# Optimization experiments

Measured on AMD Instinct MI355X. Metric: run time of the kernel, lower is better.

Reference implementation:

```python
import jax, jax.numpy as jnp
import numpy as np

D_MODEL = 1024
D_K = 64
D_V = 64
N_HEADS = 16
LN_EPS = 1e-5


def setup_inputs() -> dict:
    key = jax.random.key(0)
    ks = jax.random.split(key, 9)
    B, S = 2, 2048
    scale = 0.02
    return {
        "input_Q": jax.random.normal(ks[0], (B, S, D_MODEL), dtype=jnp.float32),
        "input_K": jax.random.normal(ks[1], (B, S, D_MODEL), dtype=jnp.float32),
        "input_V": jax.random.normal(ks[2], (B, S, D_MODEL), dtype=jnp.float32),
        "W_Q": jax.random.normal(ks[3], (D_MODEL, N_HEADS * D_K), dtype=jnp.float32) * scale,
        "W_K": jax.random.normal(ks[4], (D_MODEL, N_HEADS * D_K), dtype=jnp.float32) * scale,
        "W_V": jax.random.normal(ks[5], (D_MODEL, N_HEADS * D_V), dtype=jnp.float32) * scale,
        "W_O": jax.random.normal(ks[6], (N_HEADS * D_V, D_MODEL), dtype=jnp.float32) * scale,
        "ln_gamma": jnp.ones((D_MODEL,), dtype=jnp.float32),
        "ln_beta": jnp.zeros((D_MODEL,), dtype=jnp.float32),
    }


def reference(input_Q, input_K, input_V, W_Q, W_K, W_V, W_O, ln_gamma, ln_beta):
    B, Lq, _ = input_Q.shape
    Lk = input_K.shape[1]
    # projections -> [B, H, L, d]
    Q = (input_Q @ W_Q).reshape(B, Lq, N_HEADS, D_K).transpose(0, 2, 1, 3)
    K = (input_K @ W_K).reshape(B, Lk, N_HEADS, D_K).transpose(0, 2, 1, 3)
    V = (input_V @ W_V).reshape(B, Lk, N_HEADS, D_V).transpose(0, 2, 1, 3)
    # scores: [B, H, Lq, Lk]
    scores = jnp.einsum("bhqd,bhkd->bhqk", Q, K) / jnp.sqrt(jnp.float32(D_K))
    # NOTE: source uses nn.Softmax(dim=1) -> softmax over the HEADS axis (faithful quirk)
    attn = jax.nn.softmax(scores, axis=1)
    context = jnp.einsum("bhqk,bhkv->bhqv", attn, V)
    context = context.transpose(0, 2, 1, 3).reshape(B, Lq, N_HEADS * D_V)
    output = context @ W_O
    # residual + LayerNorm over last dim
    x = output + input_Q
    mu = jnp.mean(x, axis=-1, keepdims=True)
    var = jnp.mean(jnp.square(x - mu), axis=-1, keepdims=True)
    return (x - mu) / jnp.sqrt(var + LN_EPS) * ln_gamma + ln_beta
```

## Files before the change

### kernel.cpp

```cpp
#include <hip/hip_runtime.h>
#include <cstdint>
#include <cstddef>

#define DM 1024
#define HEADS 16
#define DHEAD 64
#define SEQ 2048
#define BATCH 2

typedef __bf16 bf16x8 __attribute__((ext_vector_type(8)));
typedef float  f32x4  __attribute__((ext_vector_type(4)));
typedef unsigned short u16;
typedef unsigned int u32;
typedef u16 u16x8 __attribute__((ext_vector_type(8)));
typedef u16 u16x4 __attribute__((ext_vector_type(4)));

__device__ __forceinline__ float bf2f(u16 u){
    union { u32 i; float f; } v; v.i = ((u32)u) << 16; return v.f;
}
__device__ __forceinline__ u16 f2bf(float f){
    union { float f; u32 i; } v; v.f = f;
    u32 r = v.i + 0x7FFF + ((v.i >> 16) & 1);
    return (u16)(r >> 16);
}
__device__ __forceinline__ u16 f2bf_rhu(float f){
    union { float f; u32 i; } v; v.f = f;
    return (u16)((v.i + 0x8000u) >> 16);
}
__device__ __forceinline__ void gload16(const u16* g, u16* l){
    __builtin_amdgcn_global_load_lds(
        (const __attribute__((address_space(1))) u32*)g,
        (__attribute__((address_space(3))) u32*)l, 16, 0, 0);
}

__global__ void k_probe(const u16* __restrict__ q, int* __restrict__ hdr){
    if (threadIdx.x == 0 && blockIdx.x == 0){
        int cnt = 0;
        for (int i = 0; i < 256; i += 2){
            int e = (q[i] >> 7) & 0xFF;
            if (e >= 90 && e <= 141) cnt++;
        }
        hdr[0] = (cnt >= 64) ? 1 : 0;
        #pragma unroll
        for (int c = 1; c <= 8; c++) hdr[c] = 0;
    }
}

__global__ __launch_bounds__(256) void k_cvt3(const void* __restrict__ s0,
                                              const void* __restrict__ s1,
                                              const void* __restrict__ s2,
                                              u16* __restrict__ dstbase,
                                              const int* __restrict__ flag, int n){
    int z = blockIdx.y;
    const void* src = (z == 0) ? s0 : ((z == 1) ? s1 : s2);
    u16* dst = dstbase + (size_t)z * n;
    int i = (blockIdx.x * 256 + threadIdx.x) * 8;
    if (i >= n) return;
    if (*flag){
        *(u16x8*)&dst[i] = *(const u16x8*)((const u16*)src + i);
    } else {
        const float* s = (const float*)src + i;
        u16x8 o;
        #pragma unroll
        for (int j = 0; j < 8; j++) o[j] = f2bf(s[j]);
        *(u16x8*)&dst[i] = o;
    }
}

__global__ void k_tcvt4(const void* __restrict__ w0, const void* __restrict__ w1,
                        const void* __restrict__ w2, const void* __restrict__ w3,
                        u16* __restrict__ dstbase,
                        const int* __restrict__ flag, int R, int C){
    __shared__ u16 tile[32][33];
    int z = blockIdx.z;
    const void* src = (z == 0) ? w0 : ((z == 1) ? w1 : ((z == 2) ? w2 : w3));
    u16* dst = dstbase + (size_t)z * R * C;
    bool isbf = (*flag != 0);
    int c0 = blockIdx.x * 32, r0 = blockIdx.y * 32;
    int tx = threadIdx.x, ty = threadIdx.y;
    #pragma unroll
    for (int i = 0; i < 32; i += 8){
        size_t idx = (size_t)(r0 + ty + i) * C + c0 + tx;
        tile[ty + i][tx] = isbf ? ((const u16*)src)[idx] : f2bf(((const float*)src)[idx]);
    }
    __syncthreads();
    #pragma unroll
    for (int i = 0; i < 32; i += 8)
        dst[(size_t)(c0 + ty + i) * R + r0 + tx] = tile[tx][ty + i];
}

__global__ void k_transpose(const u16* __restrict__ src, u16* __restrict__ dst,
                            int R, int C){
    __shared__ u16 tile[32][33];
    size_t boff = (size_t)blockIdx.z * R * C;
    src += boff; dst += boff;
    int c0 = blockIdx.x * 32, r0 = blockIdx.y * 32;
    int tx = threadIdx.x, ty = threadIdx.y;
    #pragma unroll
    for (int i = 0; i < 32; i += 8)
        tile[ty + i][tx] = src[(size_t)(r0 + ty + i) * C + c0 + tx];
    __syncthreads();
    #pragma unroll
    for (int i = 0; i < 32; i += 8)
        dst[(size_t)(c0 + ty + i) * R + r0 + tx] = tile[tx][ty + i];
}

__global__ __launch_bounds__(256, 2) void k_gemm3z(const u16* __restrict__ A0,
                                                   const u16* __restrict__ Bt0,
                                                   u16* __restrict__ C0,
                                                   size_t strA, size_t strB, size_t strC,
                                                   int M, int N, int K){
    __shared__ u16 lsA[128 * 32];
    __shared__ u16 lsB[128 * 32];
    int z = blockIdx.z;
    const u16* A  = A0  + strA * z;
    const u16* Bt = Bt0 + strB * z;
    u16* C = C0 + strC * z;
    int m0 = blockIdx.y * 128, n0 = blockIdx.x * 128;
    int t = threadIdx.x, lane = t & 63, w = t >> 6;
    int l15 = lane & 15, quad = lane >> 4;
    int wm = (w & 1) * 64, wn = (w >> 1) * 64;
    int r0 = 32 * w + (lane >> 2);
    int r1 = r0 + 16;
    int c0s = (lane & 3) ^ (r0 & 3);
    int c1s = (lane & 3) ^ (r1 & 3);
    u16* dA0 = &lsA[(32 * w) * 32];
    u16* dA1 = &lsA[(32 * w + 16) * 32];
    u16* dB0 = &lsB[(32 * w) * 32];
    u16* dB1 = &lsB[(32 * w + 16) * 32];
    f32x4 acc[4][4] = {};
    for (int k0 = 0; k0 < K; k0 += 32){
        __syncthreads();
        gload16(&A [(size_t)(m0 + r0) * K + k0 + c0s * 8], dA0);
        gload16(&A [(size_t)(m0 + r1) * K + k0 + c1s * 8], dA1);
        gload16(&Bt[(size_t)(n0 + r0) * K + k0 + c0s * 8], dB0);
        gload16(&Bt[(size_t)(n0 + r1) * K + k0 + c1s * 8], dB1);
        __syncthreads();
        bf16x8 af[4], bfr[4];
        #pragma unroll
        for (int i = 0; i < 4; i++){
            int row = wm + i * 16 + l15;
            af[i] = *(const bf16x8*)&lsA[row * 32 + ((quad ^ (row & 3)) * 8)];
        }
        #pragma unroll
        for (int j = 0; j < 4; j++){
            int row = wn + j * 16 + l15;
            bfr[j] = *(const bf16x8*)&lsB[row * 32 + ((quad ^ (row & 3)) * 8)];
        }
        #pragma unroll
        for (int i = 0; i < 4; i++)
            #pragma unroll
            for (int j = 0; j < 4; j++)
                acc[i][j] = __builtin_amdgcn_mfma_f32_16x16x32_bf16(af[i], bfr[j], acc[i][j], 0, 0, 0);
    }
    #pragma unroll
    for (int i = 0; i < 4; i++)
        #pragma unroll
        for (int j = 0; j < 4; j++)
            #pragma unroll
            for (int r = 0; r < 4; r++){
                int m = m0 + wm + i * 16 + quad * 4 + r;
                int n = n0 + wn + j * 16 + l15;
                C[(size_t)m * N + n] = f2bf(acc[i][j][r]);
            }
}

__global__ __launch_bounds__(1024, 4) void k_attn5(const u16* __restrict__ Qp,
                                                   const u16* __restrict__ Kp,
                                                   const u16* __restrict__ Vt,
                                                   u16* __restrict__ c0,
                                                   u16* __restrict__ c1,
                                                   u16* __restrict__ c2,
                                                   u16* __restrict__ c3,
                                                   int* __restrict__ cnt,
                                                   int ncomboM1, int iters){
    __shared__ u16 ebuf[2][16][64][36];
    __shared__ int s_combo, s_slot;
    int t = threadIdx.x;
    if (t == 0){
        int xcc;
        asm volatile("s_getreg_b32 %0, hwreg(HW_REG_XCC_ID)" : "=s"(xcc));
        int start = xcc & ncomboM1;
        int combo = -1, slot = -1;
        for (int a = 0; a <= ncomboM1 && combo < 0; a++){
            int c = (start + a) & ncomboM1;
            int s = atomicAdd(&cnt[c], 1);
            if (s < 32){ combo = c; slot = s; }
        }
        s_combo = combo; s_slot = slot;
    }
    __syncthreads();
    int combo = s_combo;
    if (combo < 0) return;
    int b = combo & 1, chunk = combo >> 1;
    int q0 = s_slot * 64;
    int h = t >> 6, lane = t & 63, l15 = lane & 15, quad = lane >> 4;
    u16* outp = (chunk == 0) ? c0 : ((chunk == 1) ? c1 : ((chunk == 2) ? c2 : c3));
    const float cexp = 0.125f * 1.44269504f;
    int kbeg = chunk * (iters << 5);

    bf16x8 qf[4][2];
    #pragma unroll
    for (int sub = 0; sub < 4; sub++)
        #pragma unroll
        for (int ch = 0; ch < 2; ch++)
            qf[sub][ch] = *(const bf16x8*)&Qp[((size_t)(b * SEQ + q0 + sub * 16 + l15)) * DM
                                             + h * DHEAD + ch * 32 + quad * 8];

    f32x4 oacc[4][4] = {};
    int sq = t >> 4, sku = (t & 15) * 2;

    auto score_phase = [&](int it){
        int k0 = kbeg + (it << 5), bf = it & 1;
        #pragma unroll
        for (int kt = 0; kt < 2; kt++){
            const u16* kb = Kp + ((size_t)(b * SEQ + k0 + kt * 16 + l15)) * DM + h * DHEAD + quad * 8;
            bf16x8 kf0 = *(const bf16x8*)(kb);
            bf16x8 kf1 = *(const bf16x8*)(kb + 32);
            #pragma unroll
            for (int sub = 0; sub < 4; sub++){
                f32x4 sc = {};
                sc = __builtin_amdgcn_mfma_f32_16x16x32_bf16(qf[sub][0], kf0, sc, 0, 0, 0);
                sc = __builtin_amdgcn_mfma_f32_16x16x32_bf16(qf[sub][1], kf1, sc, 0, 0, 0);
                #pragma unroll
                for (int r = 0; r < 4; r++)
                    ebuf[bf][h][sub * 16 + quad * 4 + r][kt * 16 + l15] =
                        f2bf_rhu(exp2f(sc[r] * cexp));
            }
        }
    };

    score_phase(0);
    for (int it = 0; it < iters; it++){
        int bf = it & 1;
        __syncthreads();
        if (it + 1 < iters) score_phase(it + 1);
        {
            u32 ev[16];
            float s0 = 0.f, s1 = 0.f;
            #pragma unroll
            for (int hh = 0; hh < 16; hh++){
                u32 u = *(const u32*)&ebuf[bf][hh][sq][sku];
                ev[hh] = u;
                union { u32 i; float f; } lo, hi;
                lo.i = u << 16; hi.i = u & 0xFFFF0000u;
                s0 += lo.f; s1 += hi.f;
            }
            float r0 = __builtin_amdgcn_rcpf(s0);
            float r1 = __builtin_amdgcn_rcpf(s1);
            #pragma unroll
            for (int hh = 0; hh < 16; hh++){
                union { u32 i; float f; } lo, hi, p0, p1;
                lo.i = ev[hh] << 16; hi.i = ev[hh] & 0xFFFF0000u;
                p0.f = lo.f * r0; p1.f = hi.f * r1;
                *(u32*)&ebuf[bf][hh][sq][sku] =
                    ((p0.i + 0x8000u) >> 16) | ((p1.i + 0x8000u) & 0xFFFF0000u);
            }
        }
        __syncthreads();
        int k0 = kbeg + (it << 5);
        bf16x8 pa[4];
        #pragma unroll
        for (int sub = 0; sub < 4; sub++){
            const u16* pp = &ebuf[bf][h][sub * 16 + l15][quad * 8];
            union { bf16x8 v; u16x4 q[2]; } pu;
            pu.q[0] = *(const u16x4*)pp;
            pu.q[1] = *(const u16x4*)(pp + 4);
            pa[sub] = pu.v;
        }
        #pragma unroll
        for (int vt = 0; vt < 4; vt++){
            bf16x8 vf = *(const bf16x8*)&Vt[((size_t)b * DM + h * DHEAD + vt * 16 + l15) * SEQ
                                            + k0 + quad * 8];
            #pragma unroll
            for (int sub = 0; sub < 4; sub++)
                oacc[sub][vt] = __builtin_amdgcn_mfma_f32_16x16x32_bf16(pa[sub], vf, oacc[sub][vt], 0, 0, 0);
        }
    }
    #pragma unroll
    for (int sub = 0; sub < 4; sub++)
        #pragma unroll
        for (int vt = 0; vt < 4; vt++)
            #pragma unroll
            for (int r = 0; r < 4; r++){
                int q = q0 + sub * 16 + quad * 4 + r;
                int n = h * DHEAD + vt * 16 + l15;
                outp[((size_t)b * SEQ + q) * DM + n] = f2bf(oacc[sub][vt][r]);
            }
}

__global__ __launch_bounds__(256) void k_reduce(const u16* __restrict__ a,
                                                const u16* __restrict__ b,
                                                const u16* __restrict__ c,
                                                const u16* __restrict__ d,
                                                u16* __restrict__ dst, int n, int nch){
    int i = (blockIdx.x * 256 + threadIdx.x) * 8;
    if (i >= n) return;
    u16x8 x = *(const u16x8*)&a[i];
    u16x8 y = *(const u16x8*)&b[i];
    u16x8 o;
    if (nch == 4){
        u16x8 zc = *(const u16x8*)&c[i];
        u16x8 zd = *(const u16x8*)&d[i];
        #pragma unroll
        for (int j = 0; j < 8; j++)
            o[j] = f2bf((bf2f(x[j]) + bf2f(y[j])) + (bf2f(zc[j]) + bf2f(zd[j])));
    } else {
        #pragma unroll
        for (int j = 0; j < 8; j++) o[j] = f2bf(bf2f(x[j]) + bf2f(y[j]));
    }
    *(u16x8*)&dst[i] = o;
}

__global__ __launch_bounds__(256) void k_ln(const u16* __restrict__ O,
                                            const void* __restrict__ Qin,
                                            const void* __restrict__ gamma,
                                            const void* __restrict__ beta,
                                            void* __restrict__ out,
                                            const int* __restrict__ flag){
    __shared__ float red[4][2];
    bool isbf = (*flag != 0);
    int row = blockIdx.x;
    int t = threadIdx.x;
    const u16* op = O + (size_t)row * DM;
    float xv[4];
    float s1 = 0.f, s2 = 0.f;
    #pragma unroll
    for (int i = 0; i < 4; i++){
        int idx = i * 256 + t;
        float q = isbf ? bf2f(((const u16*)Qin)[(size_t)row * DM + idx])
                       : ((const float*)Qin)[(size_t)row * DM + idx];
        float x = bf2f(op[idx]) + q;
        xv[i] = x; s1 += x; s2 += x * x;
    }
    #pragma unroll
    for (int off = 32; off; off >>= 1){
        s1 += __shfl_down(s1, off);
        s2 += __shfl_down(s2, off);
    }
    int w = t >> 6, lane = t & 63;
    if (lane == 0){ red[w][0] = s1; red[w][1] = s2; }
    __syncthreads();
    float S1 = red[0][0] + red[1][0] + red[2][0] + red[3][0];
    float S2 = red[0][1] + red[1][1] + red[2][1] + red[3][1];
    float mu  = S1 * (1.0f / DM);
    float var = S2 * (1.0f / DM) - mu * mu;
    float rstd = rsqrtf(var + 1e-5f);
    #pragma unroll
    for (int i = 0; i < 4; i++){
        int idx = i * 256 + t;
        float g = isbf ? bf2f(((const u16*)gamma)[idx]) : ((const float*)gamma)[idx];
        float bb= isbf ? bf2f(((const u16*)beta )[idx]) : ((const float*)beta )[idx];
        float y = (xv[i] - mu) * rstd * g + bb;
        if (isbf) ((u16*)out)[(size_t)row * DM + idx] = f2bf(y);
        else      ((float*)out)[(size_t)row * DM + idx] = y;
    }
}

extern "C" void kernel_launch(void* const* d_in, const int* in_sizes, int n_in,
                              void* d_out, int out_size, void* d_ws, size_t ws_size,
                              hipStream_t stream){
    (void)in_sizes; (void)n_in; (void)out_size;
    const void* inQ = d_in[0];
    const void* inK = d_in[1];
    const void* inV = d_in[2];
    const void* wQ  = d_in[3];
    const void* wK  = d_in[4];
    const void* wV  = d_in[5];
    const void* wO  = d_in[6];
    const void* gma = d_in[7];
    const void* bta = d_in[8];

    int* hdr  = (int*)d_ws;
    int* flag = hdr;
    int* cnt  = hdr + 1;
    u16* base = (u16*)d_ws + 64;

    const size_t MB1 = 1024u * 1024u;
    const size_t M4  = 4u * MB1;
    u16* Qi  = base + 0;
    u16* Ki  = base + 1 * M4;
    u16* Vi  = base + 2 * M4;
    u16* WtQ = base + 3 * M4;
    u16* WtO = WtQ + 3 * MB1;
    u16* Qp  = base + 4 * M4;
    u16* Kp  = base + 5 * M4;
    u16* Vp  = base + 6 * M4;
    u16* ext = base + 7 * M4;
    u16* Vt    = Ki;
    u16* ctxp0 = Qi;
    u16* ctxp1 = Vp;
    u16* ctxp2 = Vi;

    size_t need4 = 128 + 8 * M4 * sizeof(u16);
    int nch = (ws_size >= need4) ? 4 : 2;
    u16* ctxp3 = (nch == 4) ? ext : ctxp2;
    int ncomboM1 = 2 * nch - 1;
    int iters   = (nch == 4) ? 16 : 32;
    int ablocks = 32 * 2 * nch;

    k_probe<<<1, 64, 0, stream>>>((const u16*)inQ, hdr);

    const int nIn = BATCH * SEQ * DM;
    k_cvt3<<<dim3(nIn / 2048, 3), 256, 0, stream>>>(inQ, inK, inV, base, flag, nIn);

    k_tcvt4<<<dim3(32, 32, 4), dim3(32, 8), 0, stream>>>(wQ, wK, wV, wO, WtQ, flag, 1024, 1024);

    k_gemm3z<<<dim3(8, 32, 3), 256, 0, stream>>>(Qi, WtQ, Qp, M4, MB1, M4, 4096, 1024, 1024);

    k_transpose<<<dim3(32, 64, 2), dim3(32, 8), 0, stream>>>(Vp, Vt, 2048, 1024);

    k_attn5<<<ablocks, 1024, 0, stream>>>(Qp, Kp, Vt, ctxp0, ctxp1, ctxp2, ctxp3,
                                          cnt, ncomboM1, iters);

    k_reduce<<<nIn / 2048, 256, 0, stream>>>(ctxp0, ctxp1, ctxp2, ctxp3, ctxp0, nIn, nch);

    k_gemm3z<<<dim3(8, 32, 1), 256, 0, stream>>>(ctxp0, WtO, Qp, 0, 0, 0, 4096, 1024, 1024);

    k_ln<<<4096, 256, 0, stream>>>(Qp, inQ, gma, bta, d_out, flag);
}
```

Before: 342.9 us.

## Split head-axis softmax into denominator pass and context pass kernels

Adds a k_dsum kernel that computes, for every (query, key) pair, the reciprocal of the sum over heads of exp(score) and stores it to a bf16 global buffer. A new k_ctx kernel then recomputes the per-head scores, multiplies them by the stored reciprocal, and runs the PV MFMA. This removes the cross-head LDS exchange and the block-wide barrier-coupled score phase of the fused kernel. The price is computing QK^T twice plus writing and reading a 16 MB denominator buffer, and the path only runs when the workspace is large enough. The old fused kernel is kept as a fallback, with its next-tile score phase moved after the PV step.

```diff
diff --git a/kernel.cpp b/kernel.cpp
--- a/kernel.cpp
+++ b/kernel.cpp
@@ -42,7 +42,7 @@
         }
         hdr[0] = (cnt >= 64) ? 1 : 0;
         #pragma unroll
-        for (int c = 1; c <= 8; c++) hdr[c] = 0;
+        for (int c = 1; c <= 24; c++) hdr[c] = 0;
     }
 }
 
@@ -165,6 +165,184 @@
             }
 }
 
+__global__ __launch_bounds__(256, 2) void k_dsum(const u16* __restrict__ Qp,
+                                                 const u16* __restrict__ Kp,
+                                                 u16* __restrict__ Dg,
+                                                 int* __restrict__ cnt){
+    __shared__ u16 Klds[16 * 1024];
+    __shared__ int s_combo, s_slot;
+    int t = threadIdx.x;
+    if (t == 0){
+        int xcc;
+        asm volatile("s_getreg_b32 %0, hwreg(HW_REG_XCC_ID)" : "=s"(xcc));
+        int start = (xcc << 1) & 15;
+        int combo = -1, slot = -1;
+        for (int a = 0; a <= 15 && combo < 0; a++){
+            int c = (start + a) & 15;
+            int s = atomicAdd(&cnt[c], 1);
+            if (s < 32){ combo = c; slot = s; }
+        }
+        s_combo = combo; s_slot = slot;
+    }
+    __syncthreads();
+    int combo = s_combo;
+    if (combo < 0) return;
+    int b = combo & 1, kr = combo >> 1;
+    int kbase = kr * 256;
+    int q0 = s_slot * 64;
+    int w = t >> 6, lane = t & 63, l15 = lane & 15, quad = lane >> 4;
+    const float cexp = 0.125f * 1.44269504f;
+
+    bf16x8 qh[16][2];
+    #pragma unroll
+    for (int h = 0; h < 16; h++)
+        #pragma unroll
+        for (int ch = 0; ch < 2; ch++)
+            qh[h][ch] = *(const bf16x8*)&Qp[((size_t)(b * SEQ + q0 + w * 16 + l15)) * DM
+                                            + h * 64 + ch * 32 + quad * 8];
+
+    int rb  = l15 * 1024;
+    int sw0 = ((quad      ) ^ (l15 & 7)) * 8;
+    int sw1 = ((quad | 4  ) ^ (l15 & 7)) * 8;
+
+    for (int kt = 0; kt < 16; kt++){
+        int krow0 = b * SEQ + kbase + kt * 16;
+        __syncthreads();
+        #pragma unroll
+        for (int j = 0; j < 8; j++){
+            int u = w * 8 + j;
+            int r = u >> 1;
+            int cp = ((u & 1) << 6) | lane;
+            int cg = (cp & ~7) | ((cp & 7) ^ (r & 7));
+            gload16(&Kp[(size_t)(krow0 + r) * DM + cg * 8], &Klds[u * 512]);
+        }
+        __syncthreads();
+        f32x4 dacc = {};
+        #pragma unroll
+        for (int h = 0; h < 16; h++){
+            bf16x8 kf0 = *(const bf16x8*)&Klds[rb + h * 64 + sw0];
+            bf16x8 kf1 = *(const bf16x8*)&Klds[rb + h * 64 + sw1];
+            f32x4 sc = {};
+            sc = __builtin_amdgcn_mfma_f32_16x16x32_bf16(qh[h][0], kf0, sc, 0, 0, 0);
+            sc = __builtin_amdgcn_mfma_f32_16x16x32_bf16(qh[h][1], kf1, sc, 0, 0, 0);
+            #pragma unroll
+            for (int r = 0; r < 4; r++)
+                dacc[r] += exp2f(sc[r] * cexp);
+        }
+        #pragma unroll
+        for (int r = 0; r < 4; r++){
+            float rc = __builtin_amdgcn_rcpf(dacc[r]);
+            int q  = q0 + w * 16 + quad * 4 + r;
+            int kc = kbase + kt * 16 + (l15 ^ (quad << 2));
+            Dg[(size_t)(b * SEQ + q) * SEQ + kc] = f2bf(rc);
+        }
+    }
+}
+
+__global__ __launch_bounds__(1024, 4) void k_ctx(const u16* __restrict__ Qp,
+                                                 const u16* __restrict__ Kp,
+                                                 const u16* __restrict__ Vt,
+                                                 const u16* __restrict__ Dg,
+                                                 u16* __restrict__ c0,
+                                                 u16* __restrict__ c1,
+                                                 u16* __restrict__ c2,
+                                                 u16* __restrict__ c3,
+                                                 int* __restrict__ cnt, int iters){
+    __shared__ u16 Dlds[2][64][32];
+    __shared__ u16 scr[16][64][36];
+    __shared__ int s_combo, s_slot;
+    int t = threadIdx.x;
+    if (t == 0){
+        int xcc;
+        asm volatile("s_getreg_b32 %0, hwreg(HW_REG_XCC_ID)" : "=s"(xcc));
+        int start = xcc & 7;
+        int combo = -1, slot = -1;
+        for (int a = 0; a <= 7 && combo < 0; a++){
+            int c = (start + a) & 7;
+            int s = atomicAdd(&cnt[c], 1);
+            if (s < 32){ combo = c; slot = s; }
+        }
+        s_combo = combo; s_slot = slot;
+    }
+    __syncthreads();
+    int combo = s_combo;
+    if (combo < 0) return;
+    int b = combo & 1, chunk = combo >> 1;
+    int q0 = s_slot * 64;
+    int h = t >> 6, lane = t & 63, l15 = lane & 15, quad = lane >> 4;
+    u16* outp = (chunk == 0) ? c0 : ((chunk == 1) ? c1 : ((chunk == 2) ? c2 : c3));
+    const float cexp = 0.125f * 1.44269504f;
+    int kbeg = chunk * (iters << 5);
+
+    bf16x8 qf[4][2];
+    #pragma unroll
+    for (int sub = 0; sub < 4; sub++)
+        #pragma unroll
+        for (int ch = 0; ch < 2; ch++)
+            qf[sub][ch] = *(const bf16x8*)&Qp[((size_t)(b * SEQ + q0 + sub * 16 + l15)) * DM
+                                             + h * DHEAD + ch * 32 + quad * 8];
+
+    f32x4 oacc[4][4] = {};
+
+    auto stageD = [&](int it){
+        if (t < 256){
+            int w4 = t >> 6;
+            gload16(&Dg[(size_t)(b * SEQ + q0 + w4 * 16 + (lane >> 2)) * SEQ
+                        + kbeg + (it << 5) + (lane & 3) * 8],
+                    &Dlds[it & 1][w4 * 16][0]);
+        }
+    };
+
+    stageD(0);
+    for (int it = 0; it < iters; it++){
+        int bf = it & 1;
+        __syncthreads();
+        if (it + 1 < iters) stageD(it + 1);
+        int k0 = kbeg + (it << 5);
+        #pragma unroll
+        for (int kt = 0; kt < 2; kt++){
+            const u16* kb = Kp + ((size_t)(b * SEQ + k0 + kt * 16 + l15)) * DM + h * DHEAD + quad * 8;
+            bf16x8 kf0 = *(const bf16x8*)(kb);
+            bf16x8 kf1 = *(const bf16x8*)(kb + 32);
+            #pragma unroll
+            for (int sub = 0; sub < 4; sub++){
+                f32x4 sc = {};
+                sc = __builtin_amdgcn_mfma_f32_16x16x32_bf16(qf[sub][0], kf0, sc, 0, 0, 0);
+                sc = __builtin_amdgcn_mfma_f32_16x16x32_bf16(qf[sub][1], kf1, sc, 0, 0, 0);
+                #pragma unroll
+                for (int r = 0; r < 4; r++){
+                    float E  = exp2f(sc[r] * cexp);
+                    float rd = bf2f(Dlds[bf][sub * 16 + quad * 4 + r]
+                                        [(kt << 4) + (l15 ^ (quad << 2))]);
+                    scr[h][sub * 16 + quad * 4 + r][kt * 16 + l15] = f2bf_rhu(E * rd);
+                }
+            }
+        }
+        bf16x8 pa[4];
+        #pragma unroll
+        for (int sub = 0; sub < 4; sub++)
+            pa[sub] = *(const bf16x8*)&scr[h][sub * 16 + l15][quad * 8];
+        #pragma unroll
+        for (int vt = 0; vt < 4; vt++){
+            bf16x8 vf = *(const bf16x8*)&Vt[((size_t)b * DM + h * DHEAD + vt * 16 + l15) * SEQ
+                                            + k0 + quad * 8];
+            #pragma unroll
+            for (int sub = 0; sub < 4; sub++)
+                oacc[sub][vt] = __builtin_amdgcn_mfma_f32_16x16x32_bf16(pa[sub], vf, oacc[sub][vt], 0, 0, 0);
+        }
+    }
+    #pragma unroll
+    for (int sub = 0; sub < 4; sub++)
+        #pragma unroll
+        for (int vt = 0; vt < 4; vt++)
+            #pragma unroll
+            for (int r = 0; r < 4; r++){
+                int q = q0 + sub * 16 + quad * 4 + r;
+                int n = h * DHEAD + vt * 16 + l15;
+                outp[((size_t)b * SEQ + q) * DM + n] = f2bf(oacc[sub][vt][r]);
+            }
+}
+
 __global__ __launch_bounds__(1024, 4) void k_attn5(const u16* __restrict__ Qp,
                                                    const u16* __restrict__ Kp,
                                                    const u16* __restrict__ Vt,
@@ -234,7 +412,6 @@
     for (int it = 0; it < iters; it++){
         int bf = it & 1;
         __syncthreads();
-        if (it + 1 < iters) score_phase(it + 1);
         {
             u32 ev[16];
             float s0 = 0.f, s1 = 0.f;
@@ -276,6 +453,7 @@
             for (int sub = 0; sub < 4; sub++)
                 oacc[sub][vt] = __builtin_amdgcn_mfma_f32_16x16x32_bf16(pa[sub], vf, oacc[sub][vt], 0, 0, 0);
         }
+        if (it + 1 < iters) score_phase(it + 1);
     }
     #pragma unroll
     for (int sub = 0; sub < 4; sub++)
@@ -371,10 +549,11 @@
     const void* gma = d_in[7];
     const void* bta = d_in[8];
 
-    int* hdr  = (int*)d_ws;
-    int* flag = hdr;
-    int* cnt  = hdr + 1;
-    u16* base = (u16*)d_ws + 64;
+    int* hdr   = (int*)d_ws;
+    int* flag  = hdr;
+    int* cntA  = hdr + 1;
+    int* cntB  = hdr + 17;
+    u16* base  = (u16*)d_ws + 64;
 
     const size_t MB1 = 1024u * 1024u;
     const size_t M4  = 4u * MB1;
@@ -387,17 +566,17 @@
     u16* Kp  = base + 5 * M4;
     u16* Vp  = base + 6 * M4;
     u16* ext = base + 7 * M4;
+    u16* Dg  = base + 8 * M4;
     u16* Vt    = Ki;
     u16* ctxp0 = Qi;
     u16* ctxp1 = Vp;
     u16* ctxp2 = Vi;
 
-    size_t need4 = 128 + 8 * M4 * sizeof(u16);
-    int nch = (ws_size >= need4) ? 4 : 2;
+    size_t need4    = 128 + 8  * M4 * sizeof(u16);
+    size_t need_new = 128 + 10 * M4 * sizeof(u16);
+    bool newpath = (ws_size >= need_new);
+    int nch = (newpath || ws_size >= need4) ? 4 : 2;
     u16* ctxp3 = (nch == 4) ? ext : ctxp2;
-    int ncomboM1 = 2 * nch - 1;
-    int iters   = (nch == 4) ? 16 : 32;
-    int ablocks = 32 * 2 * nch;
 
     k_probe<<<1, 64, 0, stream>>>((const u16*)inQ, hdr);
 
@@ -410,10 +589,19 @@
 
     k_transpose<<<dim3(32, 64, 2), dim3(32, 8), 0, stream>>>(Vp, Vt, 2048, 1024);
 
-    k_attn5<<<ablocks, 1024, 0, stream>>>(Qp, Kp, Vt, ctxp0, ctxp1, ctxp2, ctxp3,
-                                          cnt, ncomboM1, iters);
-
-    k_reduce<<<nIn / 2048, 256, 0, stream>>>(ctxp0, ctxp1, ctxp2, ctxp3, ctxp0, nIn, nch);
+    if (newpath){
+        k_dsum<<<512, 256, 0, stream>>>(Qp, Kp, Dg, cntA);
+        k_ctx<<<256, 1024, 0, stream>>>(Qp, Kp, Vt, Dg, ctxp0, ctxp1, ctxp2, ctxp3,
+                                        cntB, 16);
+        k_reduce<<<nIn / 2048, 256, 0, stream>>>(ctxp0, ctxp1, ctxp2, ctxp3, ctxp0, nIn, 4);
+    } else {
+        int ncomboM1 = 2 * nch - 1;
+        int iters    = (nch == 4) ? 16 : 32;
+        int ablocks  = 32 * 2 * nch;
+        k_attn5<<<ablocks, 1024, 0, stream>>>(Qp, Kp, Vt, ctxp0, ctxp1, ctxp2, ctxp3,
+                                              cntB, ncomboM1, iters);
+        k_reduce<<<nIn / 2048, 256, 0, stream>>>(ctxp0, ctxp1, ctxp2, ctxp3, ctxp0, nIn, nch);
+    }
 
     k_gemm3z<<<dim3(8, 32, 1), 256, 0, stream>>>(ctxp0, WtO, Qp, 0, 0, 0, 4096, 1024, 1024);
 
```

Result: slower. 444.2 us (+29.5%).
